# Performance work log

Hardware: AMD Instinct MI355X
Metric: run time of the kernel (lower is better)

## Reference

```python
import jax, jax.numpy as jnp
import numpy as np

N, B, NUM_NODES, D_IN = 16384, 16, 1024, 1024
H, C = 4, 128
E = 262144


def _g(k, shape, fan_in):
    return jax.random.normal(k, shape, jnp.float32) * (1.0 / np.sqrt(fan_in))


def setup_inputs() -> dict:
    key = jax.random.key(0)
    ks = jax.random.split(key, 32)
    HC = H * C
    inp = {
        'x': jax.random.normal(ks[0], (N, D_IN), jnp.float32),
        'edge_index': jax.random.randint(ks[1], (2, E), 0, N, dtype=jnp.int64),
        'batch': jnp.repeat(jnp.arange(B, dtype=jnp.int64), NUM_NODES),
        # GATConv 1 (D_IN -> H x C, concat)
        'W1': _g(ks[2], (D_IN, HC), D_IN),
        'att_src1': _g(ks[3], (H, C), C),
        'att_dst1': _g(ks[4], (H, C), C),
        'b1': jnp.zeros((HC,), jnp.float32),
        # GATConv 2 (H*C -> H x C, concat)
        'W2': _g(ks[5], (HC, HC), HC),
        'att_src2': _g(ks[6], (H, C), C),
        'att_dst2': _g(ks[7], (H, C), C),
        'b2': jnp.zeros((HC,), jnp.float32),
        # pooling linears (HC -> 1)
        'p1w': _g(ks[8], (HC, 1), HC), 'p1b': jnp.zeros((1,), jnp.float32),
        'p2w': _g(ks[9], (HC, 1), HC), 'p2b': jnp.zeros((1,), jnp.float32),
        # layer_norm0 (applied to x2 per original code)
        'ln_g': jnp.ones((NUM_NODES,), jnp.float32),
        'ln_b': jnp.zeros((NUM_NODES,), jnp.float32),
        # encoder MLP 1024->512->256->128->64, last 64->1
        'fw1': _g(ks[10], (NUM_NODES, 512), NUM_NODES), 'fb1': jnp.zeros((512,), jnp.float32),
        'fw2': _g(ks[11], (512, 256), 512), 'fb2': jnp.zeros((256,), jnp.float32),
        'fw3': _g(ks[12], (256, 128), 256), 'fb3': jnp.zeros((128,), jnp.float32),
        'fw4': _g(ks[13], (128, 64), 128), 'fb4': jnp.zeros((64,), jnp.float32),
        'lw': _g(ks[14], (64, 1), 64), 'lb': jnp.zeros((1,), jnp.float32),
    }
    return inp


def gat_conv(x, src, dst, W, a_src, a_dst, b):
    # x: [N, F_in] -> h: [N, H, C]
    h = (x @ W).reshape(N, H, C)
    alpha_src = jnp.sum(h * a_src[None], axis=-1)  # [N, H]
    alpha_dst = jnp.sum(h * a_dst[None], axis=-1)  # [N, H]
    e = jax.nn.leaky_relu(alpha_src[src] + alpha_dst[dst], 0.2)  # [E', H]
    # segment softmax over destination neighborhoods (every node has a self loop)
    emax = jax.ops.segment_max(e, dst, num_segments=N)
    ex = jnp.exp(e - emax[dst])
    denom = jax.ops.segment_sum(ex, dst, num_segments=N)
    alpha = ex / (denom[dst] + 1e-16)  # [E', H]
    msg = h[src] * alpha[:, :, None]  # [E', H, C]
    out = jax.ops.segment_sum(msg, dst, num_segments=N)  # [N, H, C]
    return out.reshape(N, H * C) + b


def layer_norm(x, g, b, eps=1e-5):
    mu = jnp.mean(x, axis=-1, keepdims=True)
    var = jnp.var(x, axis=-1, keepdims=True)
    return (x - mu) * jax.lax.rsqrt(var + eps) * g + b


def reference(x, edge_index, batch, W1, att_src1, att_dst1, b1, W2, att_src2, att_dst2, b2,
              p1w, p1b, p2w, p2b, ln_g, ln_b, fw1, fb1, fw2, fb2, fw3, fb3, fw4, fb4, lw, lb):
    # add self loops (GATConv default)
    loops = jnp.arange(N, dtype=edge_index.dtype)
    src = jnp.concatenate([edge_index[0], loops])
    dst = jnp.concatenate([edge_index[1], loops])

    h1 = jax.nn.elu(gat_conv(x, src, dst, W1, att_src1, att_dst1, b1))
    # pool1 + to_dense_batch: batch is sorted with NUM_NODES nodes per graph -> reshape
    x1 = (h1 @ p1w + p1b).squeeze(-1).reshape(B, NUM_NODES)
    h2 = jax.nn.elu(gat_conv(h1, src, dst, W2, att_src2, att_dst2, b2))
    x2 = (h2 @ p2w + p2b).squeeze(-1).reshape(B, NUM_NODES)

    # opt.layer_norm=True; original bug: x2 normalized by layer_norm0
    x2 = layer_norm(x2, ln_g, ln_b)
    multiscale = x2  # which_layer == 'layer3'

    e = jax.nn.elu(multiscale @ fw1 + fb1)
    e = jax.nn.elu(e @ fw2 + fb2)
    e = jax.nn.elu(e @ fw3 + fb3)
    e = jax.nn.elu(e @ fw4 + fb4)
    pred = e @ lw + lb  # act_type='none' -> no activation
    return multiscale, e, pred
```

## Files before the change

kernel.cpp:

```cpp
#include <hip/hip_runtime.h>
#include <math.h>

#define NN    16384
#define DIN   1024
#define HCdim 512
#define NHEAD 4
#define NE_   262144
#define EP_   (NE_ + NN)

using short8  = __attribute__((ext_vector_type(8))) short;
using floatx4 = __attribute__((ext_vector_type(4))) float;

__device__ __forceinline__ float eluf(float x){ return x > 0.f ? x : expm1f(x); }
__device__ __forceinline__ float lrelu(float x){ return x > 0.f ? x : 0.2f * x; }
__device__ __forceinline__ float bf2f(unsigned short u){
    union { unsigned int i; float f; } c; c.i = ((unsigned int)u) << 16; return c.f;
}
__device__ __forceinline__ unsigned short f2b(float f){
    union { float f; unsigned int u; } c; c.f = f;
    unsigned int u = c.u;
    return (unsigned short)((u + 0x7FFFu + ((u >> 16) & 1u)) >> 16);
}

__global__ void k_zero_i(int* __restrict__ p, int n){
    int i = blockIdx.x * 256 + threadIdx.x;
    if (i < n) p[i] = 0;
}

__global__ void k_degree(const int* __restrict__ ei, int* __restrict__ deg){
    int i = blockIdx.x * 256 + threadIdx.x;
    if (i >= EP_) return;
    int d = (i < NE_) ? ei[NE_ + i] : (i - NE_);
    atomicAdd(&deg[d], 1);
}

__global__ __launch_bounds__(1024) void k_scan(const int* __restrict__ deg, int* __restrict__ offs){
    __shared__ int s[1024];
    int tid  = threadIdx.x;
    int base = tid * 16;
    int local[16];
    int sum = 0;
    #pragma unroll
    for (int i = 0; i < 16; i++){ local[i] = deg[base + i]; sum += local[i]; }
    s[tid] = sum;
    __syncthreads();
    for (int off = 1; off < 1024; off <<= 1){
        int v = (tid >= off) ? s[tid - off] : 0;
        __syncthreads();
        s[tid] += v;
        __syncthreads();
    }
    int run = (tid == 0) ? 0 : s[tid - 1];
    #pragma unroll
    for (int i = 0; i < 16; i++){ offs[base + i] = run; run += local[i]; }
    if (tid == 1023) offs[NN] = run;
}

__global__ void k_scatter(const int* __restrict__ ei, const int* __restrict__ offs,
                          int* __restrict__ cursor, int* __restrict__ csr){
    int i = blockIdx.x * 256 + threadIdx.x;
    if (i >= EP_) return;
    int srcv, dstv;
    if (i < NE_){ srcv = ei[i]; dstv = ei[NE_ + i]; }
    else        { srcv = dstv = i - NE_; }
    int pos = offs[dstv] + atomicAdd(&cursor[dstv], 1);
    csr[pos] = srcv;
}

__global__ __launch_bounds__(256) void k_cast_x(const float* __restrict__ x, ushort* __restrict__ xb){
    int i = blockIdx.x * 256 + threadIdx.x;
    float4 v = *(const float4*)(x + (size_t)i * 4);
    ushort4 o = { f2b(v.x), f2b(v.y), f2b(v.z), f2b(v.w) };
    *(ushort4*)(xb + (size_t)i * 4) = o;
}

__global__ __launch_bounds__(256) void k_castT(const float* __restrict__ W, ushort* __restrict__ WT,
                                               int K, int Nn, int kshift){
    int t  = blockIdx.x * 256 + threadIdx.x;
    int n  = t >> kshift;
    int kb = (t & ((1 << kshift) - 1)) * 4;
    ushort4 o;
    o.x = f2b(W[(size_t)(kb + 0) * Nn + n]);
    o.y = f2b(W[(size_t)(kb + 1) * Nn + n]);
    o.z = f2b(W[(size_t)(kb + 2) * Nn + n]);
    o.w = f2b(W[(size_t)(kb + 3) * Nn + n]);
    *(ushort4*)(WT + (size_t)n * K + kb) = o;
}

__global__ __launch_bounds__(256) void gemm_bf16(const ushort* __restrict__ A,
                                                 const ushort* __restrict__ BT,
                                                 ushort* __restrict__ C,
                                                 int M, int Nn, int K){
    __shared__ ushort As[128 * 32];
    __shared__ ushort Bs[128 * 32];
    int tid = threadIdx.x;
    int m0 = blockIdx.y * 128, n0 = blockIdx.x * 128;
    int lane = tid & 63, w = tid >> 6;
    int wm = (w >> 1) * 64, wn = (w & 1) * 64;
    int la = lane & 15, qd = lane >> 4;

    int srow = tid >> 2, schunk = (tid & 3) * 8;
    const ushort* Ag = A  + (size_t)(m0 + srow) * K + schunk;
    const ushort* Bg = BT + (size_t)(n0 + srow) * K + schunk;
    ushort* Asw = &As[srow * 32 + schunk];
    ushort* Bsw = &Bs[srow * 32 + schunk];

    floatx4 acc[4][4] = {};
    for (int k0 = 0; k0 < K; k0 += 32){
        uint4 a0 = *(const uint4*)(Ag + k0);
        uint4 a1 = *(const uint4*)(Ag + (size_t)64 * K + k0);
        uint4 b0 = *(const uint4*)(Bg + k0);
        uint4 b1 = *(const uint4*)(Bg + (size_t)64 * K + k0);
        __syncthreads();
        *(uint4*)Asw            = a0;
        *(uint4*)(Asw + 64*32)  = a1;
        *(uint4*)Bsw            = b0;
        *(uint4*)(Bsw + 64*32)  = b1;
        __syncthreads();
        short8 af[4], bf[4];
        #pragma unroll
        for (int i = 0; i < 4; i++){
            af[i] = *(const short8*)&As[(wm + i*16 + la) * 32 + qd * 8];
            bf[i] = *(const short8*)&Bs[(wn + i*16 + la) * 32 + qd * 8];
        }
        #pragma unroll
        for (int i = 0; i < 4; i++)
            #pragma unroll
            for (int j = 0; j < 4; j++)
                acc[i][j] = __builtin_amdgcn_mfma_f32_16x16x32_bf16(af[i], bf[j], acc[i][j], 0, 0, 0);
    }
    #pragma unroll
    for (int i = 0; i < 4; i++)
        #pragma unroll
        for (int j = 0; j < 4; j++){
            int col = n0 + wn + j * 16 + la;
            #pragma unroll
            for (int r = 0; r < 4; r++){
                int row = m0 + wm + i * 16 + qd * 4 + r;
                C[(size_t)row * Nn + col] = f2b(acc[i][j][r]);
            }
        }
}

__global__ __launch_bounds__(256) void k_alpha(const ushort* __restrict__ h,
    const float* __restrict__ att_s, const float* __restrict__ att_d,
    float* __restrict__ as_, float* __restrict__ ad_){
    int gt   = blockIdx.x * 256 + threadIdx.x;
    int wid  = gt >> 6;
    int lane = threadIdx.x & 63;
    int n = wid >> 2, hh = wid & 3;
    unsigned int hv = *(const unsigned int*)(h + (size_t)n * HCdim + hh * 128 + lane * 2);
    float h0 = bf2f(hv & 0xffff), h1 = bf2f(hv >> 16);
    float2 sv = *(const float2*)(att_s + hh * 128 + lane * 2);
    float2 dv = *(const float2*)(att_d + hh * 128 + lane * 2);
    float ss = h0 * sv.x + h1 * sv.y;
    float sd = h0 * dv.x + h1 * dv.y;
    #pragma unroll
    for (int off = 32; off; off >>= 1){ ss += __shfl_down(ss, off); sd += __shfl_down(sd, off); }
    if (lane == 0){ as_[n * 4 + hh] = ss; ad_[n * 4 + hh] = sd; }
}

template<bool POOL>
__global__ __launch_bounds__(128) void k_aggregate(const ushort* __restrict__ h,
    const int* __restrict__ offs, const int* __restrict__ csr,
    const float* __restrict__ as_, const float* __restrict__ ad_,
    const float* __restrict__ bias, ushort* __restrict__ out,
    const float* __restrict__ pw, const float* __restrict__ pb, float* __restrict__ x2){
    __shared__ float rpool[2];
    int n    = blockIdx.x;
    int tid  = threadIdx.x;
    int head = tid >> 5;
    int start = offs[n], end = offs[n + 1];
    float adh = ad_[n * 4 + head];
    float dsum = 0.f;
    for (int j = start + (tid & 31); j < end; j += 32){
        int s = csr[j];
        dsum += __expf(lrelu(as_[s * 4 + head] + adh));
    }
    #pragma unroll
    for (int off = 16; off; off >>= 1) dsum += __shfl_xor(dsum, off);
    float rden = 1.f / (dsum + 1e-16f);
    float a0 = 0.f, a1 = 0.f, a2 = 0.f, a3 = 0.f;
    for (int j = start; j < end; j++){
        int s = csr[j];
        float wgt = __expf(lrelu(as_[s * 4 + head] + adh)) * rden;
        uint2 hv = *(const uint2*)(h + (size_t)s * HCdim + tid * 4);
        a0 = fmaf(wgt, bf2f(hv.x & 0xffff), a0);
        a1 = fmaf(wgt, bf2f(hv.x >> 16),    a1);
        a2 = fmaf(wgt, bf2f(hv.y & 0xffff), a2);
        a3 = fmaf(wgt, bf2f(hv.y >> 16),    a3);
    }
    float4 b4 = *(const float4*)(bias + tid * 4);
    float e0 = eluf(a0 + b4.x), e1 = eluf(a1 + b4.y);
    float e2 = eluf(a2 + b4.z), e3 = eluf(a3 + b4.w);
    ushort4 o = { f2b(e0), f2b(e1), f2b(e2), f2b(e3) };
    *(ushort4*)(out + (size_t)n * HCdim + tid * 4) = o;
    if (POOL){
        float4 w4 = *(const float4*)(pw + tid * 4);
        float s = e0 * w4.x + e1 * w4.y + e2 * w4.z + e3 * w4.w;
        #pragma unroll
        for (int off = 32; off; off >>= 1) s += __shfl_down(s, off);
        if ((tid & 63) == 0) rpool[tid >> 6] = s;
        __syncthreads();
        if (tid == 0) x2[n] = rpool[0] + rpool[1] + pb[0];
    }
}

__global__ __launch_bounds__(256) void k_ln(const float* __restrict__ x2,
    const float* __restrict__ lng, const float* __restrict__ lnb,
    float* __restrict__ xnb, float* __restrict__ out){
    __shared__ float red[8];
    __shared__ float stats[2];
    int b = blockIdx.x, tid = threadIdx.x;
    float4 v = *(const float4*)(x2 + b * 1024 + tid * 4);
    float s  = v.x + v.y + v.z + v.w;
    float sq = v.x * v.x + v.y * v.y + v.z * v.z + v.w * v.w;
    #pragma unroll
    for (int off = 32; off; off >>= 1){ s += __shfl_down(s, off); sq += __shfl_down(sq, off); }
    if ((tid & 63) == 0){ red[(tid >> 6) * 2] = s; red[(tid >> 6) * 2 + 1] = sq; }
    __syncthreads();
    if (tid == 0){
        float S  = red[0] + red[2] + red[4] + red[6];
        float SQ = red[1] + red[3] + red[5] + red[7];
        float mu  = S * (1.f / 1024.f);
        float var = SQ * (1.f / 1024.f) - mu * mu;
        stats[0] = mu; stats[1] = rsqrtf(var + 1e-5f);
    }
    __syncthreads();
    float mu = stats[0], r = stats[1];
    float4 g4  = *(const float4*)(lng + tid * 4);
    float4 bb4 = *(const float4*)(lnb + tid * 4);
    float4 o;
    o.x = (v.x - mu) * r * g4.x + bb4.x;
    o.y = (v.y - mu) * r * g4.y + bb4.y;
    o.z = (v.z - mu) * r * g4.z + bb4.z;
    o.w = (v.w - mu) * r * g4.w + bb4.w;
    *(float4*)(xnb + b * 1024 + tid * 4) = o;
    *(float4*)(out + b * 1024 + tid * 4) = o;
}

template<int K, int NOUT>
__global__ __launch_bounds__(256) void k_fc(const float* __restrict__ in,
    const float* __restrict__ W, const float* __restrict__ bias, float* __restrict__ outb){
    __shared__ float xs[K];
    __shared__ float red[4][64];
    int tid = threadIdx.x;
    int b = blockIdx.y, c0 = blockIdx.x * 64;
    int tx = tid & 63, ty = tid >> 6;
    for (int i = tid * 4; i < K; i += 1024)
        *(float4*)&xs[i] = *(const float4*)(in + b * K + i);
    __syncthreads();
    const float* wp = W + (size_t)(ty * (K / 4)) * NOUT + c0 + tx;
    float a = 0.f;
    #pragma unroll 8
    for (int i = 0; i < K / 4; i++)
        a = fmaf(xs[ty * (K / 4) + i], wp[(size_t)i * NOUT], a);
    red[ty][tx] = a;
    __syncthreads();
    if (ty == 0){
        float v = red[0][tx] + red[1][tx] + red[2][tx] + red[3][tx] + bias[c0 + tx];
        outb[b * NOUT + tx + c0] = eluf(v);
    }
}

__global__ __launch_bounds__(256) void k_fc_final(const float* __restrict__ in,
    const float* __restrict__ W, const float* __restrict__ bias,
    const float* __restrict__ lw, const float* __restrict__ lb, float* __restrict__ out){
    __shared__ float xs[128];
    __shared__ float red[4][64];
    __shared__ float evs[64];
    int tid = threadIdx.x;
    int b = blockIdx.x;
    int tx = tid & 63, ty = tid >> 6;
    if (tid * 4 < 128)
        *(float4*)&xs[tid * 4] = *(const float4*)(in + b * 128 + tid * 4);
    __syncthreads();
    const float* wp = W + (size_t)(ty * 32) * 64 + tx;
    float a = 0.f;
    #pragma unroll
    for (int i = 0; i < 32; i++)
        a = fmaf(xs[ty * 32 + i], wp[(size_t)i * 64], a);
    red[ty][tx] = a;
    __syncthreads();
    if (ty == 0){
        float ev = eluf(red[0][tx] + red[1][tx] + red[2][tx] + red[3][tx] + bias[tx]);
        evs[tx] = ev;
        out[16384 + b * 64 + tx] = ev;
    }
    __syncthreads();
    if (ty == 0){
        float p = evs[tx] * lw[tx];
        #pragma unroll
        for (int off = 32; off; off >>= 1) p += __shfl_down(p, off);
        if (tx == 0) out[16384 + 1024 + b] = p + lb[0];
    }
}

extern "C" void kernel_launch(void* const* d_in, const int* in_sizes, int n_in,
                              void* d_out, int out_size, void* d_ws, size_t ws_size,
                              hipStream_t stream) {
    const float* x        = (const float*)d_in[0];
    const int*   ei       = (const int*)  d_in[1];
    const float* W1       = (const float*)d_in[3];
    const float* att_src1 = (const float*)d_in[4];
    const float* att_dst1 = (const float*)d_in[5];
    const float* b1       = (const float*)d_in[6];
    const float* W2       = (const float*)d_in[7];
    const float* att_src2 = (const float*)d_in[8];
    const float* att_dst2 = (const float*)d_in[9];
    const float* b2       = (const float*)d_in[10];
    const float* p2w      = (const float*)d_in[13];
    const float* p2b      = (const float*)d_in[14];
    const float* ln_g     = (const float*)d_in[15];
    const float* ln_b     = (const float*)d_in[16];
    const float* fw1      = (const float*)d_in[17];
    const float* fb1      = (const float*)d_in[18];
    const float* fw2      = (const float*)d_in[19];
    const float* fb2      = (const float*)d_in[20];
    const float* fw3      = (const float*)d_in[21];
    const float* fb3      = (const float*)d_in[22];
    const float* fw4      = (const float*)d_in[23];
    const float* fb4      = (const float*)d_in[24];
    const float* lw       = (const float*)d_in[25];
    const float* lb       = (const float*)d_in[26];
    float* out = (float*)d_out;

    char* w = (char*)d_ws;
    ushort* xb   = (ushort*)(w);
    ushort* h1b  = (ushort*)(w);
    ushort* h2b  = (ushort*)(w + 16777216);
    ushort* hpre = (ushort*)(w + 33554432);
    ushort* W1T  = (ushort*)(w + 50331648);
    ushort* W2T  = (ushort*)(w + 51380224);
    float* asb   = (float*)(w + 51904512);
    float* adb   = (float*)(w + 52166656);
    int*   deg   = (int*)  (w + 52428800);
    int*   cursor= (int*)  (w + 52494336);
    int*   offs  = (int*)  (w + 52559872);
    int*   csr   = (int*)  (w + 52625664);
    float* x2b   = (float*)(w + 53739776);
    float* xnb   = (float*)(w + 53805056);
    float* e1b   = (float*)(w + 53870592);
    float* e2b   = (float*)(w + 53903360);
    float* e3b   = (float*)(w + 53919744);

    k_zero_i <<<(2 * NN + 255) / 256, 256, 0, stream>>>(deg, 2 * NN);
    k_degree <<<(EP_ + 255) / 256, 256, 0, stream>>>(ei, deg);
    k_scan   <<<1, 1024, 0, stream>>>(deg, offs);
    k_scatter<<<(EP_ + 255) / 256, 256, 0, stream>>>(ei, offs, cursor, csr);

    k_cast_x<<<NN * DIN / 4 / 256, 256, 0, stream>>>(x, xb);
    k_castT <<<DIN * HCdim / 4 / 256, 256, 0, stream>>>(W1, W1T, DIN, HCdim, 8);
    k_castT <<<HCdim * HCdim / 4 / 256, 256, 0, stream>>>(W2, W2T, HCdim, HCdim, 7);

    dim3 ggrid(HCdim / 128, NN / 128);
    gemm_bf16         <<<ggrid, 256, 0, stream>>>(xb, W1T, hpre, NN, HCdim, DIN);
    k_alpha           <<<NN * NHEAD / 4, 256, 0, stream>>>(hpre, att_src1, att_dst1, asb, adb);
    k_aggregate<false><<<NN, 128, 0, stream>>>(hpre, offs, csr, asb, adb, b1, h1b,
                                               nullptr, nullptr, nullptr);
    gemm_bf16         <<<ggrid, 256, 0, stream>>>(h1b, W2T, hpre, NN, HCdim, HCdim);
    k_alpha           <<<NN * NHEAD / 4, 256, 0, stream>>>(hpre, att_src2, att_dst2, asb, adb);
    k_aggregate<true> <<<NN, 128, 0, stream>>>(hpre, offs, csr, asb, adb, b2, h2b,
                                               p2w, p2b, x2b);
    k_ln              <<<16, 256, 0, stream>>>(x2b, ln_g, ln_b, xnb, out);
    k_fc<1024, 512>   <<<dim3(8, 16), 256, 0, stream>>>(xnb, fw1, fb1, e1b);
    k_fc< 512, 256>   <<<dim3(4, 16), 256, 0, stream>>>(e1b, fw2, fb2, e2b);
    k_fc< 256, 128>   <<<dim3(2, 16), 256, 0, stream>>>(e2b, fw3, fb3, e3b);
    k_fc_final        <<<16, 256, 0, stream>>>(e3b, fw4, fb4, lw, lb, out);
}
```

Before: 396.9 us.

## Use async global-to-LDS loads in GEMM and one-wave-per-node single-pass aggregation

The GEMM now fills its shared tiles with global_load_lds 16-byte direct loads instead of staging through registers. The GAT aggregation is restructured to one 64-lane wave per node with 8 bf16 values per lane, four nodes per 256-thread block. The separate softmax-denominator pass is folded into the accumulation loop, so the division happens once at the end. This removes a second pass over the edges and the shared-memory pooling reduction. It also drops register-staged loads, at the risk of the LDS-direct load path being unsupported or ordered differently without explicit waits.

```diff
diff --git a/kernel.cpp b/kernel.cpp
--- a/kernel.cpp
+++ b/kernel.cpp
@@ -10,6 +10,10 @@
 
 using short8  = __attribute__((ext_vector_type(8))) short;
 using floatx4 = __attribute__((ext_vector_type(4))) float;
+
+typedef __attribute__((address_space(3))) unsigned int lds_uint;
+typedef const __attribute__((address_space(1))) unsigned int glb_uint;
+#define ASYNC_LD16(g, l) __builtin_amdgcn_global_load_lds((glb_uint*)(g), (lds_uint*)(l), 16, 0, 0)
 
 __device__ __forceinline__ float eluf(float x){ return x > 0.f ? x : expm1f(x); }
 __device__ __forceinline__ float lrelu(float x){ return x > 0.f ? x : 0.2f * x; }
@@ -107,15 +111,11 @@
 
     floatx4 acc[4][4] = {};
     for (int k0 = 0; k0 < K; k0 += 32){
-        uint4 a0 = *(const uint4*)(Ag + k0);
-        uint4 a1 = *(const uint4*)(Ag + (size_t)64 * K + k0);
-        uint4 b0 = *(const uint4*)(Bg + k0);
-        uint4 b1 = *(const uint4*)(Bg + (size_t)64 * K + k0);
         __syncthreads();
-        *(uint4*)Asw            = a0;
-        *(uint4*)(Asw + 64*32)  = a1;
-        *(uint4*)Bsw            = b0;
-        *(uint4*)(Bsw + 64*32)  = b1;
+        ASYNC_LD16(Ag + k0,                  Asw);
+        ASYNC_LD16(Ag + (size_t)64 * K + k0, Asw + 64 * 32);
+        ASYNC_LD16(Bg + k0,                  Bsw);
+        ASYNC_LD16(Bg + (size_t)64 * K + k0, Bsw + 64 * 32);
         __syncthreads();
         short8 af[4], bf[4];
         #pragma unroll
@@ -161,48 +161,58 @@
 }
 
 template<bool POOL>
-__global__ __launch_bounds__(128) void k_aggregate(const ushort* __restrict__ h,
+__global__ __launch_bounds__(256) void k_aggregate(const ushort* __restrict__ h,
     const int* __restrict__ offs, const int* __restrict__ csr,
     const float* __restrict__ as_, const float* __restrict__ ad_,
     const float* __restrict__ bias, ushort* __restrict__ out,
     const float* __restrict__ pw, const float* __restrict__ pb, float* __restrict__ x2){
-    __shared__ float rpool[2];
-    int n    = blockIdx.x;
-    int tid  = threadIdx.x;
-    int head = tid >> 5;
+    int wv   = threadIdx.x >> 6;
+    int lane = threadIdx.x & 63;
+    int n    = blockIdx.x * 4 + wv;
+    int head = lane >> 4;
     int start = offs[n], end = offs[n + 1];
     float adh = ad_[n * 4 + head];
     float dsum = 0.f;
-    for (int j = start + (tid & 31); j < end; j += 32){
-        int s = csr[j];
-        dsum += __expf(lrelu(as_[s * 4 + head] + adh));
-    }
-    #pragma unroll
-    for (int off = 16; off; off >>= 1) dsum += __shfl_xor(dsum, off);
-    float rden = 1.f / (dsum + 1e-16f);
-    float a0 = 0.f, a1 = 0.f, a2 = 0.f, a3 = 0.f;
+    float a0=0.f,a1=0.f,a2=0.f,a3=0.f,a4=0.f,a5=0.f,a6=0.f,a7=0.f;
     for (int j = start; j < end; j++){
         int s = csr[j];
-        float wgt = __expf(lrelu(as_[s * 4 + head] + adh)) * rden;
-        uint2 hv = *(const uint2*)(h + (size_t)s * HCdim + tid * 4);
+        float wgt = __expf(lrelu(as_[s * 4 + head] + adh));
+        dsum += wgt;
+        uint4 hv = *(const uint4*)(h + (size_t)s * HCdim + lane * 8);
         a0 = fmaf(wgt, bf2f(hv.x & 0xffff), a0);
         a1 = fmaf(wgt, bf2f(hv.x >> 16),    a1);
         a2 = fmaf(wgt, bf2f(hv.y & 0xffff), a2);
         a3 = fmaf(wgt, bf2f(hv.y >> 16),    a3);
-    }
-    float4 b4 = *(const float4*)(bias + tid * 4);
-    float e0 = eluf(a0 + b4.x), e1 = eluf(a1 + b4.y);
-    float e2 = eluf(a2 + b4.z), e3 = eluf(a3 + b4.w);
-    ushort4 o = { f2b(e0), f2b(e1), f2b(e2), f2b(e3) };
-    *(ushort4*)(out + (size_t)n * HCdim + tid * 4) = o;
+        a4 = fmaf(wgt, bf2f(hv.z & 0xffff), a4);
+        a5 = fmaf(wgt, bf2f(hv.z >> 16),    a5);
+        a6 = fmaf(wgt, bf2f(hv.w & 0xffff), a6);
+        a7 = fmaf(wgt, bf2f(hv.w >> 16),    a7);
+    }
+    float rden = 1.f / (dsum + 1e-16f);
+    float4 b0 = *(const float4*)(bias + lane * 8);
+    float4 b1 = *(const float4*)(bias + lane * 8 + 4);
+    float e0 = eluf(fmaf(a0, rden, b0.x));
+    float e1 = eluf(fmaf(a1, rden, b0.y));
+    float e2 = eluf(fmaf(a2, rden, b0.z));
+    float e3 = eluf(fmaf(a3, rden, b0.w));
+    float e4 = eluf(fmaf(a4, rden, b1.x));
+    float e5 = eluf(fmaf(a5, rden, b1.y));
+    float e6 = eluf(fmaf(a6, rden, b1.z));
+    float e7 = eluf(fmaf(a7, rden, b1.w));
+    uint4 o;
+    o.x = (unsigned)f2b(e0) | ((unsigned)f2b(e1) << 16);
+    o.y = (unsigned)f2b(e2) | ((unsigned)f2b(e3) << 16);
+    o.z = (unsigned)f2b(e4) | ((unsigned)f2b(e5) << 16);
+    o.w = (unsigned)f2b(e6) | ((unsigned)f2b(e7) << 16);
+    *(uint4*)(out + (size_t)n * HCdim + lane * 8) = o;
     if (POOL){
-        float4 w4 = *(const float4*)(pw + tid * 4);
-        float s = e0 * w4.x + e1 * w4.y + e2 * w4.z + e3 * w4.w;
+        float4 w0 = *(const float4*)(pw + lane * 8);
+        float4 w1 = *(const float4*)(pw + lane * 8 + 4);
+        float s = e0*w0.x + e1*w0.y + e2*w0.z + e3*w0.w
+                + e4*w1.x + e5*w1.y + e6*w1.z + e7*w1.w;
         #pragma unroll
         for (int off = 32; off; off >>= 1) s += __shfl_down(s, off);
-        if ((tid & 63) == 0) rpool[tid >> 6] = s;
-        __syncthreads();
-        if (tid == 0) x2[n] = rpool[0] + rpool[1] + pb[0];
+        if (lane == 0) x2[n] = s + pb[0];
     }
 }
 
@@ -356,12 +366,12 @@
     dim3 ggrid(HCdim / 128, NN / 128);
     gemm_bf16         <<<ggrid, 256, 0, stream>>>(xb, W1T, hpre, NN, HCdim, DIN);
     k_alpha           <<<NN * NHEAD / 4, 256, 0, stream>>>(hpre, att_src1, att_dst1, asb, adb);
-    k_aggregate<false><<<NN, 128, 0, stream>>>(hpre, offs, csr, asb, adb, b1, h1b,
-                                               nullptr, nullptr, nullptr);
+    k_aggregate<false><<<NN / 4, 256, 0, stream>>>(hpre, offs, csr, asb, adb, b1, h1b,
+                                                   nullptr, nullptr, nullptr);
     gemm_bf16         <<<ggrid, 256, 0, stream>>>(h1b, W2T, hpre, NN, HCdim, HCdim);
     k_alpha           <<<NN * NHEAD / 4, 256, 0, stream>>>(hpre, att_src2, att_dst2, asb, adb);
-    k_aggregate<true> <<<NN, 128, 0, stream>>>(hpre, offs, csr, asb, adb, b2, h2b,
-                                               p2w, p2b, x2b);
+    k_aggregate<true> <<<NN / 4, 256, 0, stream>>>(hpre, offs, csr, asb, adb, b2, h2b,
+                                                   p2w, p2b, x2b);
     k_ln              <<<16, 256, 0, stream>>>(x2b, ln_g, ln_b, xnb, out);
     k_fc<1024, 512>   <<<dim3(8, 16), 256, 0, stream>>>(xnb, fw1, fb1, e1b);
     k_fc< 512, 256>   <<<dim3(4, 16), 256, 0, stream>>>(e1b, fw2, fb2, e2b);
```

Measured after the change: 392.5 us. No clear change (-1.1%).
